# Performance work log

Measured on AMD Instinct MI355X. Metric: run time of the kernel, lower is better.

The kernel has to match this reference:

```python
import jax, jax.numpy as jnp
import numpy as np

B, S, D, H, DFF, L, R, V = 2, 1024, 1024, 16, 4096, 2, 3, 32000
HD = D // H


def layer_norm(x, g, b, eps=1e-5):
    mu = jnp.mean(x, axis=-1, keepdims=True)
    var = jnp.var(x, axis=-1, keepdims=True)
    return (x - mu) / jnp.sqrt(var + eps) * g + b


def recursion_block(x, mask, Wqkv, bqkv, Wo, bo, W1, b1, W2, b2, ln1_g, ln1_b, ln2_g, ln2_b):
    # shared pre-LN transformer stack of L layers, applied once per recursion step
    Bc, Sc, _ = x.shape
    scale = 1.0 / np.sqrt(HD).astype(np.float32)
    for l in range(L):
        h = layer_norm(x, ln1_g[l], ln1_b[l])
        qkv = h @ Wqkv[l] + bqkv[l]
        q, k, v = jnp.split(qkv, 3, axis=-1)
        q = q.reshape(Bc, Sc, H, HD).transpose(0, 2, 1, 3)
        k = k.reshape(Bc, Sc, H, HD).transpose(0, 2, 1, 3)
        v = v.reshape(Bc, Sc, H, HD).transpose(0, 2, 1, 3)
        scores = jnp.einsum('bhqd,bhkd->bhqk', q, k) * scale + mask
        attn = jax.nn.softmax(scores, axis=-1)
        o = jnp.einsum('bhqk,bhkd->bhqd', attn, v).transpose(0, 2, 1, 3).reshape(Bc, Sc, D)
        x = x + o @ Wo[l] + bo[l]
        h2 = layer_norm(x, ln2_g[l], ln2_b[l])
        x = x + jax.nn.gelu(h2 @ W1[l] + b1[l]) @ W2[l] + b2[l]
    return x


def setup_inputs() -> dict:
    key = jax.random.key(0)
    ks = jax.random.split(key, 12)
    n = lambda k, shape: (jax.random.normal(k, shape, jnp.float32) * 0.02)
    return {
        'input_ids': jax.random.randint(ks[0], (B, S), 0, V),
        'token_embed': n(ks[1], (V, D)),
        'pos_embed': n(ks[2], (S, D)),
        'Wqkv': n(ks[3], (L, D, 3 * D)), 'bqkv': jnp.zeros((L, 3 * D), jnp.float32),
        'Wo': n(ks[4], (L, D, D)), 'bo': jnp.zeros((L, D), jnp.float32),
        'W1': n(ks[5], (L, D, DFF)), 'b1': jnp.zeros((L, DFF), jnp.float32),
        'W2': n(ks[6], (L, DFF, D)), 'b2': jnp.zeros((L, D), jnp.float32),
        'ln1_g': jnp.ones((L, D), jnp.float32), 'ln1_b': jnp.zeros((L, D), jnp.float32),
        'ln2_g': jnp.ones((L, D), jnp.float32), 'ln2_b': jnp.zeros((L, D), jnp.float32),
        'final_g': jnp.ones((D,), jnp.float32), 'final_b': jnp.zeros((D,), jnp.float32),
        'Wr': n(ks[7], (D, R)), 'br': jnp.zeros((R,), jnp.float32),
    }


def reference(input_ids, token_embed, pos_embed, Wqkv, bqkv, Wo, bo, W1, b1, W2, b2,
              ln1_g, ln1_b, ln2_g, ln2_b, final_g, final_b, Wr, br):
    h = token_embed[input_ids] + pos_embed[None, :, :]            # [B,S,D]
    mask = jnp.where(jnp.tril(jnp.ones((S, S), bool)), 0.0, -jnp.inf)[None, None]  # [1,1,S,S]
    # token-choice router on detached hidden states
    rlogits = jax.lax.stop_gradient(h) @ Wr + br                  # [B,S,R]
    probs = jax.nn.softmax(rlogits, axis=-1)
    depth_map = jnp.argmax(rlogits, axis=-1) + 1                  # depths in 1..R
    importance = probs.mean(axis=(0, 1))
    router_loss = R * jnp.sum(importance ** 2)                    # load-balance aux loss
    res = h
    for step in range(R):
        step_mask = depth_map >= step + 1                         # [B,S] bool
        upd = recursion_block(res, mask, Wqkv, bqkv, Wo, bo, W1, b1, W2, b2,
                              ln1_g, ln1_b, ln2_g, ln2_b)
        res = jnp.where(step_mask[..., None], upd, res)
    hf = layer_norm(res, final_g, final_b)
    logits = hf @ token_embed.T                                   # tied lm_head
    return logits, depth_map, router_loss
```

## Files before the change

### kernel.cpp

```cpp
#include <hip/hip_runtime.h>
#include <hip/hip_bf16.h>

#define DD 1024
#define SS 1024
#define BB 2
#define HH 16
#define DFFN 4096
#define LLAYERS 2
#define RSTEPS 3
#define VV 32000
#define NTOK (BB*SS)

typedef __attribute__((ext_vector_type(8))) short s16x8;
typedef __attribute__((ext_vector_type(8))) __bf16 bf16x8;
typedef __attribute__((ext_vector_type(4))) float f32x4;

__device__ __forceinline__ unsigned short f2bf(float f) {
  unsigned int u = __float_as_uint(f);
  u += 0x7FFFu + ((u >> 16) & 1u);
  return (unsigned short)(u >> 16);
}

__device__ __forceinline__ f32x4 mfma16(s16x8 a, s16x8 b, f32x4 c) {
  return __builtin_amdgcn_mfma_f32_16x16x32_bf16(
      __builtin_bit_cast(bf16x8, a), __builtin_bit_cast(bf16x8, b), c, 0, 0, 0);
}

__device__ __forceinline__ void gload16(const unsigned short* g, unsigned short* l) {
  __builtin_amdgcn_global_load_lds(
      (const __attribute__((address_space(1))) unsigned int*)(const void*)g,
      (__attribute__((address_space(3))) unsigned int*)(void*)l, 16, 0, 0);
}

#define BAR()  asm volatile("s_barrier" ::: "memory")
#define LGK0() do { asm volatile("s_waitcnt lgkmcnt(0)" ::: "memory"); \
                    __builtin_amdgcn_sched_barrier(0); } while (0)
#define VM4()  asm volatile("s_waitcnt vmcnt(4)" ::: "memory")
#define VM0()  asm volatile("s_waitcnt vmcnt(0)" ::: "memory")

template<int N> __device__ __forceinline__ void vmw() {
  if constexpr (N == 0) asm volatile("s_waitcnt vmcnt(0)" ::: "memory");
  else if constexpr (N == 3) asm volatile("s_waitcnt vmcnt(3)" ::: "memory");
  else if constexpr (N == 4) asm volatile("s_waitcnt vmcnt(4)" ::: "memory");
  else if constexpr (N == 6) asm volatile("s_waitcnt vmcnt(6)" ::: "memory");
  else if constexpr (N == 8) asm volatile("s_waitcnt vmcnt(8)" ::: "memory");
}

__global__ __launch_bounds__(256) void prep_all_kernel(
    const float* __restrict__ Wqkv, const float* __restrict__ Wo,
    const float* __restrict__ W1, const float* __restrict__ W2,
    const float* __restrict__ te,
    unsigned short* __restrict__ WqkvT, unsigned short* __restrict__ WoT,
    unsigned short* __restrict__ W1T, unsigned short* __restrict__ W2T,
    unsigned short* __restrict__ teb,
    const int* __restrict__ ids, const float* __restrict__ pe,
    const float* __restrict__ Wr, const float* __restrict__ br,
    float* __restrict__ res, float* __restrict__ probs,
    float* __restrict__ depth_ws, float* __restrict__ out_depth) {
  const int bid = blockIdx.x;
  const int tid = threadIdx.x;
  __shared__ unsigned short t[64][68];
  __shared__ float red[4][3];
  if (bid >= 22144) {
    int row = bid - 22144;
    int s = row & (SS - 1);
    int id = ids[row];
    int d = tid * 4;
    float4 a = *(const float4*)(te + (long)id * DD + d);
    float4 p = *(const float4*)(pe + (long)s * DD + d);
    float4 o; o.x = a.x + p.x; o.y = a.y + p.y; o.z = a.z + p.z; o.w = a.w + p.w;
    *(float4*)(res + (long)row * DD + d) = o;
    float a0 = 0.f, a1 = 0.f, a2 = 0.f;
    float hv[4] = {o.x, o.y, o.z, o.w};
#pragma unroll
    for (int j = 0; j < 4; ++j) {
      int dd = d + j;
      a0 += hv[j] * Wr[dd * 3 + 0];
      a1 += hv[j] * Wr[dd * 3 + 1];
      a2 += hv[j] * Wr[dd * 3 + 2];
    }
    for (int off = 32; off; off >>= 1) {
      a0 += __shfl_down(a0, off);
      a1 += __shfl_down(a1, off);
      a2 += __shfl_down(a2, off);
    }
    int wave = tid >> 6;
    if ((tid & 63) == 0) { red[wave][0] = a0; red[wave][1] = a1; red[wave][2] = a2; }
    __syncthreads();
    if (tid == 0) {
      a0 = red[0][0] + red[1][0] + red[2][0] + red[3][0] + br[0];
      a1 = red[0][1] + red[1][1] + red[2][1] + red[3][1] + br[1];
      a2 = red[0][2] + red[1][2] + red[2][2] + red[3][2] + br[2];
      float m = fmaxf(a0, fmaxf(a1, a2));
      float e0 = expf(a0 - m), e1 = expf(a1 - m), e2 = expf(a2 - m);
      float inv = 1.f / (e0 + e1 + e2);
      probs[row * 3 + 0] = e0 * inv;
      probs[row * 3 + 1] = e1 * inv;
      probs[row * 3 + 2] = e2 * inv;
      int am = 0; float bv = a0;
      if (a1 > bv) { bv = a1; am = 1; }
      if (a2 > bv) { bv = a2; am = 2; }
      float dm = (float)(am + 1);
      depth_ws[row] = dm;
      out_depth[row] = dm;
    }
    return;
  }
  if (bid >= 6144) {
    long i = ((long)(bid - 6144) * 256 + tid) * 8;
    float4 v0 = *(const float4*)(te + i);
    float4 v1 = *(const float4*)(te + i + 4);
    ushort4 a, b;
    a.x = f2bf(v0.x); a.y = f2bf(v0.y); a.z = f2bf(v0.z); a.w = f2bf(v0.w);
    b.x = f2bf(v1.x); b.y = f2bf(v1.y); b.z = f2bf(v1.z); b.w = f2bf(v1.w);
    *(ushort4*)(teb + i) = a;
    *(ushort4*)(teb + i + 4) = b;
    return;
  }
  const float* src; unsigned short* dst; int Kd, Nd, local;
  if (bid < 1536) {
    int l = (bid >= 768);
    local = bid - l * 768;
    src = Wqkv + (long)l * DD * 3 * DD; dst = WqkvT + (long)l * 3 * DD * DD;
    Kd = DD; Nd = 3 * DD;
  } else if (bid < 2048) {
    int l = (bid - 1536) >> 8; local = (bid - 1536) & 255;
    src = Wo + (long)l * DD * DD; dst = WoT + (long)l * DD * DD;
    Kd = DD; Nd = DD;
  } else if (bid < 4096) {
    int l = (bid - 2048) >> 10; local = (bid - 2048) & 1023;
    src = W1 + (long)l * DD * DFFN; dst = W1T + (long)l * DFFN * DD;
    Kd = DD; Nd = DFFN;
  } else {
    int l = (bid - 4096) >> 10; local = (bid - 4096) & 1023;
    src = W2 + (long)l * DFFN * DD; dst = W2T + (long)l * DD * DFFN;
    Kd = DFFN; Nd = DD;
  }
  const int tn = Nd >> 6;
  const int n0 = (local % tn) * 64, k0 = (local / tn) * 64;
#pragma unroll
  for (int c = 0; c < 4; ++c) {
    int p = tid + c * 256;
    int kr = p >> 4, nc = (p & 15) * 4;
    float4 v = *(const float4*)(src + (long)(k0 + kr) * Nd + n0 + nc);
    t[nc + 0][kr] = f2bf(v.x);
    t[nc + 1][kr] = f2bf(v.y);
    t[nc + 2][kr] = f2bf(v.z);
    t[nc + 3][kr] = f2bf(v.w);
  }
  __syncthreads();
#pragma unroll
  for (int c = 0; c < 4; ++c) {
    int p = tid + c * 256;
    int nr = p >> 4, kc = (p & 15) * 4;
    ushort4 o;
    o.x = t[nr][kc]; o.y = t[nr][kc + 1]; o.z = t[nr][kc + 2]; o.w = t[nr][kc + 3];
    *(ushort4*)(dst + (long)(n0 + nr) * Kd + k0 + kc) = o;
  }
}

__global__ __launch_bounds__(256) void router_finalize_kernel(
    const float* __restrict__ probs, float* __restrict__ out_loss) {
  __shared__ float red[256][3];
  int t = threadIdx.x;
  float s0 = 0.f, s1 = 0.f, s2 = 0.f;
  for (int r = t; r < NTOK; r += 256) {
    s0 += probs[r * 3 + 0]; s1 += probs[r * 3 + 1]; s2 += probs[r * 3 + 2];
  }
  red[t][0] = s0; red[t][1] = s1; red[t][2] = s2;
  __syncthreads();
  for (int off = 128; off; off >>= 1) {
    if (t < off) {
      red[t][0] += red[t + off][0];
      red[t][1] += red[t + off][1];
      red[t][2] += red[t + off][2];
    }
    __syncthreads();
  }
  if (t == 0) {
    float i0 = red[0][0] / NTOK, i1 = red[0][1] / NTOK, i2 = red[0][2] / NTOK;
    out_loss[0] = (float)RSTEPS * (i0 * i0 + i1 * i1 + i2 * i2);
  }
}

__global__ __launch_bounds__(256) void ln_kernel(
    const float* __restrict__ x, const float* __restrict__ g,
    const float* __restrict__ b, unsigned short* __restrict__ y) {
  int row = blockIdx.x;
  int t = threadIdx.x;
  float4 v = *(const float4*)(x + (long)row * DD + t * 4);
  float s = v.x + v.y + v.z + v.w;
  float q = v.x * v.x + v.y * v.y + v.z * v.z + v.w * v.w;
  for (int off = 32; off; off >>= 1) {
    s += __shfl_down(s, off);
    q += __shfl_down(q, off);
  }
  __shared__ float rs[4], rq[4];
  int wave = t >> 6;
  if ((t & 63) == 0) { rs[wave] = s; rq[wave] = q; }
  __syncthreads();
  float S_ = rs[0] + rs[1] + rs[2] + rs[3];
  float Q_ = rq[0] + rq[1] + rq[2] + rq[3];
  float mu = S_ * (1.f / DD);
  float var = Q_ * (1.f / DD) - mu * mu;
  float rstd = rsqrtf(var + 1e-5f);
  int d = t * 4;
  float4 gg = *(const float4*)(g + d);
  float4 bb = *(const float4*)(b + d);
  ushort4 ov;
  ov.x = f2bf((v.x - mu) * rstd * gg.x + bb.x);
  ov.y = f2bf((v.y - mu) * rstd * gg.y + bb.y);
  ov.z = f2bf((v.z - mu) * rstd * gg.z + bb.z);
  ov.w = f2bf((v.w - mu) * rstd * gg.w + bb.w);
  *(ushort4*)(y + (long)row * DD + d) = ov;
}

__device__ __forceinline__ void stageA8(unsigned short* S, int buf, int qm,
    const unsigned short* A, int lda, long m0, int kt, int tid) {
  unsigned short* dst = S + buf * 32768 + qm * 8192;
#pragma unroll
  for (int c = 0; c < 2; ++c) {
    int idx = tid + c * 512;
    int L = (idx << 4) ^ (((idx >> 5) & 1) << 5);
    int band = L >> 13, row = (L >> 7) & 63, kel = (L & 127) >> 1;
    gload16(A + (m0 + band * 128 + qm * 64 + row) * (long)lda + kt * 64 + kel,
            dst + idx * 8);
  }
}

__device__ __forceinline__ void stageB8(unsigned short* S, int buf, int qn,
    const unsigned short* Bt, int ldb, long n0, int kt, int tid) {
  unsigned short* dst = S + buf * 32768 + 16384 + qn * 8192;
#pragma unroll
  for (int c = 0; c < 2; ++c) {
    int idx = tid + c * 512;
    int L = (idx << 4) ^ (((idx >> 5) & 1) << 5);
    int band = L >> 12, row = (L >> 7) & 31, kel = (L & 127) >> 1;
    gload16(Bt + (n0 + band * 64 + qn * 32 + row) * (long)ldb + kt * 64 + kel,
            dst + idx * 8);
  }
}

__device__ __forceinline__ void read_af8(const unsigned short* S, int base,
    int wm, int l16, int g, s16x8 af[2][4]) {
  const int swz = ((l16 >> 2) & 1) << 5;
#pragma unroll
  for (int kk = 0; kk < 2; ++kk)
#pragma unroll
    for (int mf = 0; mf < 4; ++mf) {
      int L = (wm * 8192 + (mf * 16 + l16) * 128 + (kk * 32 + g * 8) * 2) ^ swz;
      af[kk][mf] = *(const s16x8*)(S + base + (L >> 1));
    }
}

__device__ __forceinline__ void read_bf8(const unsigned short* S, int base,
    int wn, int l16, int g, s16x8 bf[2][2]) {
  const int swz = ((l16 >> 2) & 1) << 5;
#pragma unroll
  for (int kk = 0; kk < 2; ++kk)
#pragma unroll
    for (int nf = 0; nf < 2; ++nf) {
      int L = (wn * 4096 + (nf * 16 + l16) * 128 + (kk * 32 + g * 8) * 2) ^ swz;
      bf[kk][nf] = *(const s16x8*)(S + base + (L >> 1));
    }
}

template<int QM, int QN>
__device__ __forceinline__ void do_mfma8(f32x4 acc[8][4],
    const s16x8 af[2][4], const s16x8 bf[2][2]) {
  __builtin_amdgcn_s_setprio(1);
#pragma unroll
  for (int kk = 0; kk < 2; ++kk)
#pragma unroll
    for (int mf = 0; mf < 4; ++mf)
#pragma unroll
      for (int nf = 0; nf < 2; ++nf)
        acc[QM * 4 + mf][QN * 2 + nf] =
            mfma16(af[kk][mf], bf[kk][nf], acc[QM * 4 + mf][QN * 2 + nf]);
  __builtin_amdgcn_s_setprio(0);
}

template<int CBF16, int BIAS, int GELU_ACT>
__global__ __launch_bounds__(512, 1) void gemm256_kernel(
    const unsigned short* __restrict__ A, int lda,
    const unsigned short* __restrict__ Bt, int ldb,
    void* __restrict__ Cv, int ldc,
    const float* __restrict__ bias, int K, int Mblocks) {
  __shared__ unsigned short S[65536];
  const int tid = threadIdx.x;
  const int lane = tid & 63, wave = tid >> 6;
  const int g = lane >> 4, l16 = lane & 15;
  const int wm = wave >> 2, wn = wave & 3;
  const int nwg = gridDim.x * gridDim.y;
  const int orig = blockIdx.x + blockIdx.y * gridDim.x;
  const int q = nwg >> 3, r = nwg & 7;
  const int xcd = orig & 7, loc = orig >> 3;
  const int wgid = (xcd < r ? xcd * (q + 1) : r * (q + 1) + (xcd - r) * q) + loc;
  const long m0 = (long)(wgid % Mblocks) * 256;
  const long n0 = (long)(wgid / Mblocks) * 256;

  f32x4 acc[8][4] = {};
  s16x8 af[2][4], bf[2][2];
  const int NI = K >> 7;

  stageA8(S, 0, 0, A, lda, m0, 0, tid);
  stageA8(S, 0, 1, A, lda, m0, 0, tid);
  stageB8(S, 0, 0, Bt, ldb, n0, 0, tid);
  stageB8(S, 0, 1, Bt, ldb, n0, 0, tid);
  stageA8(S, 1, 0, A, lda, m0, 1, tid);
  stageB8(S, 1, 1, Bt, ldb, n0, 1, tid);
  VM4(); BAR();

  for (int i = 0; i < NI; ++i) {
    const int kt1 = 2 * i + 1, kt2 = 2 * i + 2, kt3 = 2 * i + 3;
    const bool more = (i + 1 < NI);
    read_af8(S, 0, wm, l16, g, af);
    read_bf8(S, 16384, wn, l16, g, bf);
    stageA8(S, 1, 1, A, lda, m0, kt1, tid);
    BAR(); LGK0();
    do_mfma8<0, 0>(acc, af, bf);
    BAR();
    read_bf8(S, 16384 + 8192, wn, l16, g, bf);
    stageB8(S, 1, 0, Bt, ldb, n0, kt1, tid);
    BAR(); LGK0();
    do_mfma8<0, 1>(acc, af, bf);
    BAR();
    read_af8(S, 8192, wm, l16, g, af);
    if (more) stageA8(S, 0, 0, A, lda, m0, kt2, tid);
    BAR(); LGK0();
    do_mfma8<1, 1>(acc, af, bf);
    BAR();
    read_bf8(S, 16384, wn, l16, g, bf);
    if (more) stageB8(S, 0, 1, Bt, ldb, n0, kt2, tid);
    BAR(); LGK0();
    do_mfma8<1, 0>(acc, af, bf);
    if (more) { VM4(); } else { VM0(); }
    BAR();
    read_af8(S, 32768, wm, l16, g, af);
    read_bf8(S, 32768 + 16384, wn, l16, g, bf);
    if (more) stageA8(S, 0, 1, A, lda, m0, kt2, tid);
    BAR(); LGK0();
    do_mfma8<0, 0>(acc, af, bf);
    BAR();
    read_bf8(S, 32768 + 16384 + 8192, wn, l16, g, bf);
    if (more) stageB8(S, 0, 0, Bt, ldb, n0, kt2, tid);
    BAR(); LGK0();
    do_mfma8<0, 1>(acc, af, bf);
    BAR();
    read_af8(S, 32768 + 8192, wm, l16, g, af);
    if (more) stageA8(S, 1, 0, A, lda, m0, kt3, tid);
    BAR(); LGK0();
    do_mfma8<1, 1>(acc, af, bf);
    BAR();
    read_bf8(S, 32768 + 16384, wn, l16, g, bf);
    if (more) stageB8(S, 1, 1, Bt, ldb, n0, kt3, tid);
    BAR(); LGK0();
    do_mfma8<1, 0>(acc, af, bf);
    VM4(); BAR();
  }

#pragma unroll
  for (int mf = 0; mf < 8; ++mf) {
#pragma unroll
    for (int nf = 0; nf < 4; ++nf) {
      long row0 = m0 + wm * 128 + mf * 16 + g * 4;
      long col = n0 + wn * 64 + nf * 16 + l16;
      float bv = BIAS ? bias[col] : 0.f;
#pragma unroll
      for (int rr = 0; rr < 4; ++rr) {
        float v = acc[mf][nf][rr] + bv;
        if (GELU_ACT) {
          float x3 = v * v * v;
          v = 0.5f * v * (1.f + tanhf(0.7978845608028654f * (v + 0.044715f * x3)));
        }
        if (CBF16) ((unsigned short*)Cv)[(row0 + rr) * (long)ldc + col] = f2bf(v);
        else       ((float*)Cv)[(row0 + rr) * (long)ldc + col] = v;
      }
    }
  }
}

template<int BN, int DEPTH, int CBF16, int BIAS, int RESID, int GELU_ACT,
         int SELW, int QKVW>
__global__ __launch_bounds__(512) void gemm_db_kernel(
    const unsigned short* __restrict__ A, int lda,
    const unsigned short* __restrict__ Bt, int ldb,
    void* __restrict__ Cv, int ldc,
    const float* __restrict__ bias,
    const float* __restrict__ resid, int ldr,
    const float* __restrict__ depth_ws, float stepf,
    unsigned short* __restrict__ vtw,
    int K) {
  constexpr int WN = BN / 2;
  constexpr int NR = WN / 16;
  constexpr int ACH = 2;
  constexpr int BCH = BN / 64;
  constexpr int LPT = ACH + BCH;
  __shared__ unsigned short As[DEPTH][128 * 64];
  __shared__ unsigned short Bs[DEPTH][BN * 64];
  const int tid = threadIdx.x;
  const int lane = tid & 63, wave = tid >> 6;
  const int g = lane >> 4, l16 = lane & 15;
  const int wr = wave >> 1, wc = wave & 1;
  int lin = blockIdx.x + blockIdx.y * gridDim.x;
  int per = (gridDim.x * gridDim.y) >> 3;
  int v = (lin & 7) * per + (lin >> 3);
  const long m0 = (long)(v % gridDim.y) * 128;
  const long n0 = (long)(v / gridDim.y) * BN;
  f32x4 acc[2][NR] = {};
  const int NT = K >> 6;

  auto stage = [&](int buf, int kt) {
    const int k0 = kt * 64;
#pragma unroll
    for (int c = 0; c < ACH; ++c) {
      int p = tid + c * 512;
      int L = (p << 4) ^ (((p >> 5) & 1) << 5);
      int row = L >> 7, kel = (L & 127) >> 1;
      gload16(A + (m0 + row) * (long)lda + k0 + kel, &As[buf][p * 8]);
    }
#pragma unroll
    for (int c = 0; c < BCH; ++c) {
      int p = tid + c * 512;
      int L = (p << 4) ^ (((p >> 5) & 1) << 5);
      int row = L >> 7, kel = (L & 127) >> 1;
      gload16(Bt + (n0 + row) * (long)ldb + k0 + kel, &Bs[buf][p * 8]);
    }
  };

#pragma unroll
  for (int j = 0; j < DEPTH - 1; ++j) stage(j, j);

  int cur = 0;
  const int swz = ((l16 >> 2) & 1) << 5;
  for (int kt = 0; kt < NT; ++kt) {
    const int rem = NT - 1 - kt;
    if (rem >= DEPTH - 1) {
      int tgt = cur + DEPTH - 1; if (tgt >= DEPTH) tgt -= DEPTH;
      stage(tgt, kt + DEPTH - 1);
      vmw<(DEPTH - 1) * LPT>();
    } else if (DEPTH == 3 && rem == 1) {
      vmw<LPT>();
    } else {
      vmw<0>();
    }
    BAR();
#pragma unroll
    for (int kk = 0; kk < 2; ++kk) {
      s16x8 af[2], bf[NR];
#pragma unroll
      for (int m = 0; m < 2; ++m) {
        int L = (((wr * 32 + m * 16 + l16) << 7) + ((kk * 32 + g * 8) << 1)) ^ swz;
        af[m] = *(const s16x8*)&As[cur][L >> 1];
      }
#pragma unroll
      for (int n = 0; n < NR; ++n) {
        int L = (((wc * WN + n * 16 + l16) << 7) + ((kk * 32 + g * 8) << 1)) ^ swz;
        bf[n] = *(const s16x8*)&Bs[cur][L >> 1];
      }
#pragma unroll
      for (int m = 0; m < 2; ++m)
#pragma unroll
        for (int n = 0; n < NR; ++n)
          acc[m][n] = mfma16(af[m], bf[n], acc[m][n]);
    }
    BAR();
    ++cur; if (cur == DEPTH) cur = 0;
  }

  const bool vblk = QKVW && (n0 >= 2048);
#pragma unroll
  for (int m = 0; m < 2; ++m) {
#pragma unroll
    for (int n = 0; n < NR; ++n) {
      long row_base = m0 + wr * 32 + m * 16 + g * 4;
      long col = n0 + wc * WN + n * 16 + l16;
      float bv = BIAS ? bias[col] : 0.f;
      float vv4[4];
#pragma unroll
      for (int r = 0; r < 4; ++r) {
        long row = row_base + r;
        float vv = acc[m][n][r] + bv;
        if (RESID) vv += resid[row * (long)ldr + col];
        if (GELU_ACT) {
          float x3 = vv * vv * vv;
          vv = 0.5f * vv * (1.f + tanhf(0.7978845608028654f * (vv + 0.044715f * x3)));
        }
        vv4[r] = vv;
      }
      if (QKVW && vblk) {
        int rel = (int)col - 2048;
        int h = rel >> 6, d = rel & 63;
        int b = (int)(row_base >> 10);
        int s = (int)(row_base & 1023);
        ushort4 o;
        o.x = f2bf(vv4[0]); o.y = f2bf(vv4[1]);
        o.z = f2bf(vv4[2]); o.w = f2bf(vv4[3]);
        *(ushort4*)(vtw + (((long)(b * 16 + h) * 64 + d) * SS + s)) = o;
      } else {
#pragma unroll
        for (int r = 0; r < 4; ++r) {
          long row = row_base + r;
          if (SELW) {
            if (depth_ws[row] >= stepf)
              ((float*)Cv)[row * (long)ldc + col] = vv4[r];
          } else if (CBF16) {
            ((unsigned short*)Cv)[row * (long)ldc + col] = f2bf(vv4[r]);
          } else {
            ((float*)Cv)[row * (long)ldc + col] = vv4[r];
          }
        }
      }
    }
  }
}

__global__ __launch_bounds__(512) void attn_kernel(
    const unsigned short* __restrict__ qkv,
    const unsigned short* __restrict__ vt,
    unsigned short* __restrict__ o) {
  __shared__ unsigned short Ks[2][64 * 64];
  __shared__ unsigned short Vs[2][64 * 64];
  __shared__ unsigned short Pl[8][16][72];
  const int qb = gridDim.x - 1 - blockIdx.x;
  const int bh = blockIdx.y;
  const int b = bh >> 4, h = bh & 15;
  const int tid = threadIdx.x, wave = tid >> 6, lane = tid & 63;
  const int g = lane >> 4, l16 = lane & 15;
  const float NEG_INF = -__builtin_inff();
  const int q0 = qb * 128;
  const int qrw = q0 + wave * 16;
  const long rowbase = (long)b * SS;
  const unsigned short* kbase = qkv + rowbase * 3072 + 1024 + h * 64;
  const unsigned short* vbase = vt + (long)bh * 64 * SS;

  const unsigned short* qptr = qkv + (rowbase + qrw + l16) * 3072 + h * 64;
  s16x8 qf0 = *(const s16x8*)(qptr + g * 8);
  s16x8 qf1 = *(const s16x8*)(qptr + 32 + g * 8);

  f32x4 oacc[4] = {};
  float mrun = NEG_INF, lrun = 0.f;

  const int ntile = q0 / 64 + 2;

  {
    int r = tid >> 3;
    int bo = (tid & 7) * 16;
    int sw = (bo ^ ((r & 7) << 4)) >> 1;
    gload16(kbase + (long)r * 3072 + sw, &Ks[0][tid * 8]);
    gload16(vbase + (long)r * SS + 0 + sw, &Vs[0][tid * 8]);
  }
  asm volatile("s_waitcnt vmcnt(0)" ::: "memory");
  __syncthreads();

  for (int t = 0; t < ntile; ++t) {
    const int cur = t & 1;
    const int kv0 = t * 64;
    const unsigned short* ks_cur = &Ks[cur][0];
    const unsigned short* vs_cur = &Vs[cur][0];
    if (t + 1 < ntile) {
      const int kvn = kv0 + 64;
      int r = tid >> 3;
      int bo = (tid & 7) * 16;
      int sw = (bo ^ ((r & 7) << 4)) >> 1;
      gload16(kbase + (long)(kvn + r) * 3072 + sw, &Ks[cur ^ 1][tid * 8]);
      gload16(vbase + (long)r * SS + kvn + sw, &Vs[cur ^ 1][tid * 8]);
    }
    f32x4 accs[4] = {};
#pragma unroll
    for (int ks = 0; ks < 2; ++ks) {
#pragma unroll
      for (int kvb = 0; kvb < 4; ++kvb) {
        int row = kvb * 16 + l16;
        int bo = ((ks * 64 + g * 16) ^ ((l16 & 7) << 4)) >> 1;
        s16x8 kf = *(const s16x8*)&ks_cur[row * 64 + bo];
        accs[kvb] = mfma16(kf, ks ? qf1 : qf0, accs[kvb]);
      }
    }
    const bool needmask = (kv0 + 63 > qrw);
    const int qabs = qrw + l16;
    float sv[4][4];
    float mloc = NEG_INF;
#pragma unroll
    for (int kvb = 0; kvb < 4; ++kvb) {
#pragma unroll
      for (int r = 0; r < 4; ++r) {
        float vv = accs[kvb][r] * 0.125f;
        if (needmask) {
          int kva = kv0 + kvb * 16 + g * 4 + r;
          if (kva > qabs) vv = NEG_INF;
        }
        sv[kvb][r] = vv;
        mloc = fmaxf(mloc, vv);
      }
    }
    mloc = fmaxf(mloc, __shfl_xor(mloc, 16));
    mloc = fmaxf(mloc, __shfl_xor(mloc, 32));
    float mnew = fmaxf(mrun, mloc);
    float alpha = __expf(mrun - mnew);
    float lsum = 0.f;
#pragma unroll
    for (int kvb = 0; kvb < 4; ++kvb) {
      float p0 = __expf(sv[kvb][0] - mnew);
      float p1 = __expf(sv[kvb][1] - mnew);
      float p2 = __expf(sv[kvb][2] - mnew);
      float p3 = __expf(sv[kvb][3] - mnew);
      lsum += (p0 + p1) + (p2 + p3);
      unsigned int w0 = (unsigned)f2bf(p0) | ((unsigned)f2bf(p1) << 16);
      unsigned int w1 = (unsigned)f2bf(p2) | ((unsigned)f2bf(p3) << 16);
      uint2 pw; pw.x = w0; pw.y = w1;
      *(uint2*)&Pl[wave][l16][kvb * 16 + g * 4] = pw;
    }
    lsum += __shfl_xor(lsum, 16);
    lsum += __shfl_xor(lsum, 32);
    lrun = lrun * alpha + lsum;
    mrun = mnew;
    float mult[4];
#pragma unroll
    for (int r = 0; r < 4; ++r) mult[r] = __shfl(alpha, g * 4 + r);
#pragma unroll
    for (int nd = 0; nd < 4; ++nd)
#pragma unroll
      for (int r = 0; r < 4; ++r) oacc[nd][r] *= mult[r];
#pragma unroll
    for (int kh = 0; kh < 2; ++kh) {
      s16x8 pa = *(const s16x8*)&Pl[wave][l16][kh * 32 + g * 8];
#pragma unroll
      for (int nd = 0; nd < 4; ++nd) {
        int row = nd * 16 + l16;
        int bo = ((kh * 64 + g * 16) ^ ((l16 & 7) << 4)) >> 1;
        s16x8 vf = *(const s16x8*)&vs_cur[row * 64 + bo];
        oacc[nd] = mfma16(pa, vf, oacc[nd]);
      }
    }
    asm volatile("s_waitcnt vmcnt(0)" ::: "memory");
    __syncthreads();
  }
  unsigned short* ob = o + (rowbase + qrw) * 1024 + h * 64;
#pragma unroll
  for (int r = 0; r < 4; ++r) {
    float lr = __shfl(lrun, g * 4 + r);
    float inv = 1.f / lr;
#pragma unroll
    for (int nd = 0; nd < 4; ++nd)
      ob[(long)(g * 4 + r) * 1024 + nd * 16 + l16] = f2bf(oacc[nd][r] * inv);
  }
}

extern "C" void kernel_launch(void* const* d_in, const int* in_sizes, int n_in,
                              void* d_out, int out_size, void* d_ws, size_t ws_size,
                              hipStream_t stream) {
  (void)in_sizes; (void)n_in; (void)out_size; (void)ws_size;
  const int*   ids  = (const int*)d_in[0];
  const float* te   = (const float*)d_in[1];
  const float* pe   = (const float*)d_in[2];
  const float* Wqkv = (const float*)d_in[3];
  const float* bqkv = (const float*)d_in[4];
  const float* Wo   = (const float*)d_in[5];
  const float* bo   = (const float*)d_in[6];
  const float* W1   = (const float*)d_in[7];
  const float* b1   = (const float*)d_in[8];
  const float* W2   = (const float*)d_in[9];
  const float* b2   = (const float*)d_in[10];
  const float* ln1g = (const float*)d_in[11];
  const float* ln1b = (const float*)d_in[12];
  const float* ln2g = (const float*)d_in[13];
  const float* ln2b = (const float*)d_in[14];
  const float* fing = (const float*)d_in[15];
  const float* finb = (const float*)d_in[16];
  const float* Wr   = (const float*)d_in[17];
  const float* br   = (const float*)d_in[18];

  float* logits    = (float*)d_out;
  float* out_depth = logits + (long)NTOK * VV;
  float* out_loss  = out_depth + NTOK;

  char* w = (char*)d_ws;
  float* res            = (float*)w;          w += (long)NTOK * DD * 4;
  float* x              = (float*)w;          w += (long)NTOK * DD * 4;
  unsigned short* hbuf  = (unsigned short*)w; w += (long)NTOK * DD * 2;
  unsigned short* qkvb  = (unsigned short*)w; w += (long)NTOK * 3 * DD * 2;
  unsigned short* obuf  = (unsigned short*)w; w += (long)NTOK * DD * 2;
  unsigned short* ffn1  = (unsigned short*)w; w += (long)NTOK * DFFN * 2;
  unsigned short* vtb   = (unsigned short*)w; w += (long)BB * HH * 64 * SS * 2;
  float* probs          = (float*)w;          w += (long)NTOK * 3 * 4;
  float* depth_ws       = (float*)w;          w += (long)NTOK * 4;
  unsigned short* WqkvT = (unsigned short*)w; w += (long)LLAYERS * 3 * DD * DD * 2;
  unsigned short* WoT   = (unsigned short*)w; w += (long)LLAYERS * DD * DD * 2;
  unsigned short* W1T   = (unsigned short*)w; w += (long)LLAYERS * DFFN * DD * 2;
  unsigned short* W2T   = (unsigned short*)w; w += (long)LLAYERS * DD * DFFN * 2;
  unsigned short* teb   = (unsigned short*)w; w += (long)VV * DD * 2;

  prep_all_kernel<<<6144 + 16000 + NTOK, 256, 0, stream>>>(
      Wqkv, Wo, W1, W2, te, WqkvT, WoT, W1T, W2T, teb,
      ids, pe, Wr, br, res, probs, depth_ws, out_depth);
  router_finalize_kernel<<<1, 256, 0, stream>>>(probs, out_loss);

  for (int step = 0; step < RSTEPS; ++step) {
    for (int l = 0; l < LLAYERS; ++l) {
      const float* xin = (l == 0) ? res : x;
      ln_kernel<<<NTOK, 256, 0, stream>>>(xin, ln1g + l * DD, ln1b + l * DD, hbuf);
      gemm_db_kernel<128, 2, 1, 1, 0, 0, 0, 1>
          <<<dim3(3 * DD / 128, NTOK / 128), 512, 0, stream>>>(
          hbuf, DD, WqkvT + (long)l * 3 * DD * DD, DD, qkvb, 3 * DD,
          bqkv + (long)l * 3 * DD, nullptr, 0, nullptr, 0.f, vtb, DD);
      attn_kernel<<<dim3(SS / 128, BB * HH), 512, 0, stream>>>(qkvb, vtb, obuf);
      gemm_db_kernel<64, 3, 0, 1, 1, 0, 0, 0>
          <<<dim3(DD / 64, NTOK / 128), 512, 0, stream>>>(
          obuf, DD, WoT + (long)l * DD * DD, DD, x, DD,
          bo + (long)l * DD, xin, DD, nullptr, 0.f, nullptr, DD);
      ln_kernel<<<NTOK, 256, 0, stream>>>(x, ln2g + l * DD, ln2b + l * DD, hbuf);
      gemm_db_kernel<128, 2, 1, 1, 0, 1, 0, 0>
          <<<dim3(DFFN / 128, NTOK / 128), 512, 0, stream>>>(
          hbuf, DD, W1T + (long)l * DFFN * DD, DD, ffn1, DFFN,
          b1 + (long)l * DFFN, nullptr, 0, nullptr, 0.f, nullptr, DD);
      if (l == 0) {
        gemm_db_kernel<64, 3, 0, 1, 1, 0, 0, 0>
            <<<dim3(DD / 64, NTOK / 128), 512, 0, stream>>>(
            ffn1, DFFN, W2T + (long)l * DD * DFFN, DFFN, x, DD,
            b2 + (long)l * DD, x, DD, nullptr, 0.f, nullptr, DFFN);
      } else {
        gemm_db_kernel<64, 3, 0, 1, 1, 0, 1, 0>
            <<<dim3(DD / 64, NTOK / 128), 512, 0, stream>>>(
            ffn1, DFFN, W2T + (long)l * DD * DFFN, DFFN, res, DD,
            b2 + (long)l * DD, x, DD, depth_ws, (float)(step + 1), nullptr, DFFN);
      }
    }
  }
  ln_kernel<<<NTOK, 256, 0, stream>>>(res, fing, finb, hbuf);
  gemm256_kernel<0, 0, 0><<<dim3(VV / 256, NTOK / 256), 512, 0, stream>>>(
      hbuf, DD, teb, DD, logits, VV, nullptr, DD, NTOK / 256);
}
```

Before: 1.217 ms.

## Compact active tokens for last-layer post-attention work in later recursion steps

Adds a compaction kernel that builds index lists of tokens whose routed depth reaches steps 2 and 3. In the last layer of those steps, the Wo projection gathers only the active rows, and the following LN, FFN1 and FFN2 run only on the compacted count, with blocks past the count exiting early. FFN2 then scatters results back into the residual. This removes post-attention GEMM work for tokens whose result would be discarded. The cost is gathered row loads, a single-block serial prefix scan, and an extra activation buffer.

```diff
diff --git a/kernel.cpp b/kernel.cpp
--- a/kernel.cpp
+++ b/kernel.cpp
@@ -183,10 +183,49 @@
   }
 }
 
+__global__ __launch_bounds__(256) void compact_kernel(
+    const float* __restrict__ depth_ws, int* __restrict__ idx1,
+    int* __restrict__ idx2, int* __restrict__ cnts) {
+  __shared__ int c1[256], c2[256];
+  __shared__ int tot[2];
+  int t = threadIdx.x;
+  int l1 = 0, l2 = 0;
+  for (int j = 0; j < 8; ++j) {
+    float d = depth_ws[t * 8 + j];
+    l1 += (d >= 2.f); l2 += (d >= 3.f);
+  }
+  c1[t] = l1; c2[t] = l2;
+  __syncthreads();
+  if (t == 0) {
+    int a = 0, b = 0;
+    for (int i = 0; i < 256; ++i) {
+      int t1 = c1[i]; c1[i] = a; a += t1;
+      int t2 = c2[i]; c2[i] = b; b += t2;
+    }
+    tot[0] = a; tot[1] = b;
+    cnts[0] = a; cnts[1] = b;
+  }
+  __syncthreads();
+  int o1 = c1[t], o2 = c2[t];
+  for (int j = 0; j < 8; ++j) {
+    int r = t * 8 + j;
+    float d = depth_ws[r];
+    if (d >= 2.f) idx1[o1++] = r;
+    if (d >= 3.f) idx2[o2++] = r;
+  }
+  __syncthreads();
+  for (int i = t; i < NTOK; i += 256) {
+    if (i >= tot[0]) idx1[i] = 0;
+    if (i >= tot[1]) idx2[i] = 0;
+  }
+}
+
 __global__ __launch_bounds__(256) void ln_kernel(
     const float* __restrict__ x, const float* __restrict__ g,
-    const float* __restrict__ b, unsigned short* __restrict__ y) {
+    const float* __restrict__ b, unsigned short* __restrict__ y,
+    const int* __restrict__ cntp) {
   int row = blockIdx.x;
+  if (cntp && row >= *cntp) return;
   int t = threadIdx.x;
   float4 v = *(const float4*)(x + (long)row * DD + t * 4);
   float s = v.x + v.y + v.z + v.w;
@@ -381,7 +420,7 @@
 }
 
 template<int BN, int DEPTH, int CBF16, int BIAS, int RESID, int GELU_ACT,
-         int SELW, int QKVW>
+         int SELW, int QKVW, int GMODE>
 __global__ __launch_bounds__(512) void gemm_db_kernel(
     const unsigned short* __restrict__ A, int lda,
     const unsigned short* __restrict__ Bt, int ldb,
@@ -390,6 +429,7 @@
     const float* __restrict__ resid, int ldr,
     const float* __restrict__ depth_ws, float stepf,
     unsigned short* __restrict__ vtw,
+    const int* __restrict__ idxs, const int* __restrict__ cntp,
     int K) {
   constexpr int WN = BN / 2;
   constexpr int NR = WN / 16;
@@ -407,8 +447,20 @@
   int v = (lin & 7) * per + (lin >> 3);
   const long m0 = (long)(v % gridDim.y) * 128;
   const long n0 = (long)(v / gridDim.y) * BN;
+  int cnt = 0;
+  if (GMODE) { cnt = *cntp; if (m0 >= cnt) return; }
   f32x4 acc[2][NR] = {};
   const int NT = K >> 6;
+
+  int arow[ACH];
+#pragma unroll
+  for (int c = 0; c < ACH; ++c) {
+    int p = tid + c * 512;
+    int L = (p << 4) ^ (((p >> 5) & 1) << 5);
+    int row = L >> 7;
+    if (GMODE == 1) arow[c] = idxs[m0 + row];
+    else            arow[c] = (int)(m0 + row);
+  }
 
   auto stage = [&](int buf, int kt) {
     const int k0 = kt * 64;
@@ -416,8 +468,8 @@
     for (int c = 0; c < ACH; ++c) {
       int p = tid + c * 512;
       int L = (p << 4) ^ (((p >> 5) & 1) << 5);
-      int row = L >> 7, kel = (L & 127) >> 1;
-      gload16(A + (m0 + row) * (long)lda + k0 + kel, &As[buf][p * 8]);
+      int kel = (L & 127) >> 1;
+      gload16(A + (long)arow[c] * lda + k0 + kel, &As[buf][p * 8]);
     }
 #pragma unroll
     for (int c = 0; c < BCH; ++c) {
@@ -481,7 +533,10 @@
       for (int r = 0; r < 4; ++r) {
         long row = row_base + r;
         float vv = acc[m][n][r] + bv;
-        if (RESID) vv += resid[row * (long)ldr + col];
+        if (RESID) {
+          if (GMODE == 1) vv += resid[(long)idxs[row] * ldr + col];
+          else            vv += resid[row * (long)ldr + col];
+        }
         if (GELU_ACT) {
           float x3 = vv * vv * vv;
           vv = 0.5f * vv * (1.f + tanhf(0.7978845608028654f * (vv + 0.044715f * x3)));
@@ -501,7 +556,10 @@
 #pragma unroll
         for (int r = 0; r < 4; ++r) {
           long row = row_base + r;
-          if (SELW) {
+          if (GMODE == 3) {
+            if (row < cnt)
+              ((float*)Cv)[(long)idxs[row] * ldc + col] = vv4[r];
+          } else if (SELW) {
             if (depth_ws[row] >= stepf)
               ((float*)Cv)[row * (long)ldc + col] = vv4[r];
           } else if (CBF16) {
@@ -678,6 +736,7 @@
   char* w = (char*)d_ws;
   float* res            = (float*)w;          w += (long)NTOK * DD * 4;
   float* x              = (float*)w;          w += (long)NTOK * DD * 4;
+  float* xc             = (float*)w;          w += (long)NTOK * DD * 4;
   unsigned short* hbuf  = (unsigned short*)w; w += (long)NTOK * DD * 2;
   unsigned short* qkvb  = (unsigned short*)w; w += (long)NTOK * 3 * DD * 2;
   unsigned short* obuf  = (unsigned short*)w; w += (long)NTOK * DD * 2;
@@ -685,6 +744,8 @@
   unsigned short* vtb   = (unsigned short*)w; w += (long)BB * HH * 64 * SS * 2;
   float* probs          = (float*)w;          w += (long)NTOK * 3 * 4;
   float* depth_ws       = (float*)w;          w += (long)NTOK * 4;
+  int* idxb             = (int*)w;            w += (long)2 * NTOK * 4;
+  int* cnts             = (int*)w;            w += 64;
   unsigned short* WqkvT = (unsigned short*)w; w += (long)LLAYERS * 3 * DD * DD * 2;
   unsigned short* WoT   = (unsigned short*)w; w += (long)LLAYERS * DD * DD * 2;
   unsigned short* W1T   = (unsigned short*)w; w += (long)LLAYERS * DFFN * DD * 2;
@@ -695,39 +756,67 @@
       Wqkv, Wo, W1, W2, te, WqkvT, WoT, W1T, W2T, teb,
       ids, pe, Wr, br, res, probs, depth_ws, out_depth);
   router_finalize_kernel<<<1, 256, 0, stream>>>(probs, out_loss);
+  compact_kernel<<<1, 256, 0, stream>>>(depth_ws, idxb, idxb + NTOK, cnts);
 
   for (int step = 0; step < RSTEPS; ++step) {
     for (int l = 0; l < LLAYERS; ++l) {
       const float* xin = (l == 0) ? res : x;
-      ln_kernel<<<NTOK, 256, 0, stream>>>(xin, ln1g + l * DD, ln1b + l * DD, hbuf);
-      gemm_db_kernel<128, 2, 1, 1, 0, 0, 0, 1>
+      ln_kernel<<<NTOK, 256, 0, stream>>>(xin, ln1g + l * DD, ln1b + l * DD, hbuf,
+                                          nullptr);
+      gemm_db_kernel<128, 2, 1, 1, 0, 0, 0, 1, 0>
           <<<dim3(3 * DD / 128, NTOK / 128), 512, 0, stream>>>(
           hbuf, DD, WqkvT + (long)l * 3 * DD * DD, DD, qkvb, 3 * DD,
-          bqkv + (long)l * 3 * DD, nullptr, 0, nullptr, 0.f, vtb, DD);
+          bqkv + (long)l * 3 * DD, nullptr, 0, nullptr, 0.f, vtb,
+          nullptr, nullptr, DD);
       attn_kernel<<<dim3(SS / 128, BB * HH), 512, 0, stream>>>(qkvb, vtb, obuf);
-      gemm_db_kernel<64, 3, 0, 1, 1, 0, 0, 0>
-          <<<dim3(DD / 64, NTOK / 128), 512, 0, stream>>>(
-          obuf, DD, WoT + (long)l * DD * DD, DD, x, DD,
-          bo + (long)l * DD, xin, DD, nullptr, 0.f, nullptr, DD);
-      ln_kernel<<<NTOK, 256, 0, stream>>>(x, ln2g + l * DD, ln2b + l * DD, hbuf);
-      gemm_db_kernel<128, 2, 1, 1, 0, 1, 0, 0>
-          <<<dim3(DFFN / 128, NTOK / 128), 512, 0, stream>>>(
-          hbuf, DD, W1T + (long)l * DFFN * DD, DD, ffn1, DFFN,
-          b1 + (long)l * DFFN, nullptr, 0, nullptr, 0.f, nullptr, DD);
-      if (l == 0) {
-        gemm_db_kernel<64, 3, 0, 1, 1, 0, 0, 0>
+      if (l == 1 && step > 0) {
+        const int* idx = idxb + (step - 1) * NTOK;
+        const int* cnt = cnts + (step - 1);
+        gemm_db_kernel<64, 3, 0, 1, 1, 0, 0, 0, 1>
             <<<dim3(DD / 64, NTOK / 128), 512, 0, stream>>>(
-            ffn1, DFFN, W2T + (long)l * DD * DFFN, DFFN, x, DD,
-            b2 + (long)l * DD, x, DD, nullptr, 0.f, nullptr, DFFN);
-      } else {
-        gemm_db_kernel<64, 3, 0, 1, 1, 0, 1, 0>
+            obuf, DD, WoT + (long)l * DD * DD, DD, xc, DD,
+            bo + (long)l * DD, x, DD, nullptr, 0.f, nullptr, idx, cnt, DD);
+        ln_kernel<<<NTOK, 256, 0, stream>>>(xc, ln2g + l * DD, ln2b + l * DD, hbuf,
+                                            cnt);
+        gemm_db_kernel<128, 2, 1, 1, 0, 1, 0, 0, 2>
+            <<<dim3(DFFN / 128, NTOK / 128), 512, 0, stream>>>(
+            hbuf, DD, W1T + (long)l * DFFN * DD, DD, ffn1, DFFN,
+            b1 + (long)l * DFFN, nullptr, 0, nullptr, 0.f, nullptr,
+            nullptr, cnt, DD);
+        gemm_db_kernel<64, 3, 0, 1, 1, 0, 0, 0, 3>
             <<<dim3(DD / 64, NTOK / 128), 512, 0, stream>>>(
             ffn1, DFFN, W2T + (long)l * DD * DFFN, DFFN, res, DD,
-            b2 + (long)l * DD, x, DD, depth_ws, (float)(step + 1), nullptr, DFFN);
+            b2 + (long)l * DD, xc, DD, nullptr, 0.f, nullptr, idx, cnt, DFFN);
+      } else {
+        gemm_db_kernel<64, 3, 0, 1, 1, 0, 0, 0, 0>
+            <<<dim3(DD / 64, NTOK / 128), 512, 0, stream>>>(
+            obuf, DD, WoT + (long)l * DD * DD, DD, x, DD,
+            bo + (long)l * DD, xin, DD, nullptr, 0.f, nullptr,
+            nullptr, nullptr, DD);
+        ln_kernel<<<NTOK, 256, 0, stream>>>(x, ln2g + l * DD, ln2b + l * DD, hbuf,
+                                            nullptr);
+        gemm_db_kernel<128, 2, 1, 1, 0, 1, 0, 0, 0>
+            <<<dim3(DFFN / 128, NTOK / 128), 512, 0, stream>>>(
+            hbuf, DD, W1T + (long)l * DFFN * DD, DD, ffn1, DFFN,
+            b1 + (long)l * DFFN, nullptr, 0, nullptr, 0.f, nullptr,
+            nullptr, nullptr, DD);
+        if (l == 0) {
+          gemm_db_kernel<64, 3, 0, 1, 1, 0, 0, 0, 0>
+              <<<dim3(DD / 64, NTOK / 128), 512, 0, stream>>>(
+              ffn1, DFFN, W2T + (long)l * DD * DFFN, DFFN, x, DD,
+              b2 + (long)l * DD, x, DD, nullptr, 0.f, nullptr,
+              nullptr, nullptr, DFFN);
+        } else {
+          gemm_db_kernel<64, 3, 0, 1, 1, 0, 1, 0, 0>
+              <<<dim3(DD / 64, NTOK / 128), 512, 0, stream>>>(
+              ffn1, DFFN, W2T + (long)l * DD * DFFN, DFFN, res, DD,
+              b2 + (long)l * DD, x, DD, depth_ws, 1.f, nullptr,
+              nullptr, nullptr, DFFN);
+        }
       }
     }
   }
-  ln_kernel<<<NTOK, 256, 0, stream>>>(res, fing, finb, hbuf);
+  ln_kernel<<<NTOK, 256, 0, stream>>>(res, fing, finb, hbuf, nullptr);
   gemm256_kernel<0, 0, 0><<<dim3(VV / 256, NTOK / 256), 512, 0, stream>>>(
       hbuf, DD, teb, DD, logits, VV, nullptr, DD, NTOK / 256);
 }
```

New measurement: 1.248 ms. 2.5% more time.
